# Performance work log

Hardware: AMD Instinct MI355X
Metric: run time of the kernel (lower is better)

## Reference

```python
import jax, jax.numpy as jnp
import numpy as np

# Norse-style LIF constants (LIFParameters defaults, method='super', alpha=100)
DT = 0.001
TAU_SYN_INV = 200.0
TAU_MEM_INV = 100.0
V_TH = 1.0
V_LEAK = 0.0
V_RESET = 0.0
ALPHA = 100.0

@jax.custom_vjp
def heaviside(x):
    return (x > 0).astype(x.dtype)

def _heaviside_fwd(x):
    return heaviside(x), x

def _heaviside_bwd(x, g):
    # SuperSpike surrogate: 1 / (alpha*|x| + 1)^2
    return (g / (ALPHA * jnp.abs(x) + 1.0) ** 2,)

heaviside.defvjp(_heaviside_fwd, _heaviside_bwd)

def lif_step(v, i, inp_cur):
    # explicit-Euler LIF: membrane decays toward leak driven by synaptic current,
    # synaptic current decays, spikes reset membrane, input arrives as current jump
    v_dec = v + DT * TAU_MEM_INV * ((V_LEAK - v) + i)
    i_dec = i * (1.0 - DT * TAU_SYN_INV)
    z = heaviside(v_dec - V_TH)
    v_new = (1.0 - z) * v_dec + z * V_RESET
    i_new = i_dec + inp_cur
    return z, v_new, i_new

def li_step(v, i, inp_cur):
    # leaky integrator (non-spiking readout)
    v_new = v + DT * TAU_MEM_INV * ((V_LEAK - v) + i)
    i_new = i * (1.0 - DT * TAU_SYN_INV) + inp_cur
    return v_new, i_new


def setup_inputs() -> dict:
    key = jax.random.key(0)
    k1, k2, k3 = jax.random.split(key, 3)
    T, B = 64, 128
    FS2, H1, HC, OC, OUT = 4096, 2048, 2, 4, 10
    spl1, spl2 = FS2 // HC, H1 // OC
    x = jax.random.uniform(k1, (T, B, FS2), dtype=jnp.float32)
    w_hidden = jax.random.normal(k2, (HC, spl1, H1), dtype=jnp.float32) / np.sqrt(spl1)
    w_out = jax.random.normal(k3, (OC, spl2, OUT), dtype=jnp.float32) / np.sqrt(spl2)
    return {"x": x, "w_hidden": w_hidden, "w_out": w_out}


def reference(x, w_hidden, w_out):
    T, B, FS2 = x.shape
    HC, SPL1, H1 = w_hidden.shape
    OC, SPL2, OUT = w_out.shape
    f32 = x.dtype

    def step(carry, x_t):
        vdh, idh, vsh, ish, vdo, ido, vso, iso = carry
        # split input across hidden dendritic channels: [HC, B, SPL1]
        zc = x_t.reshape(B, HC, SPL1).transpose(1, 0, 2)
        cur_h = jnp.einsum('cbi,cio->cbo', zc, w_hidden)      # [HC, B, H1]
        s_d, vdh, idh = lif_step(vdh, idh, cur_h)             # dendritic spikes
        z_s, vsh, ish = lif_step(vsh, ish, s_d.sum(0))        # somatic spikes [B, H1]
        # split hidden spikes across output dendritic channels: [OC, B, SPL2]
        zo = z_s.reshape(B, OC, SPL2).transpose(1, 0, 2)
        cur_o = jnp.einsum('cbi,cio->cbo', zo, w_out)         # [OC, B, OUT]
        s_o, vdo, ido = lif_step(vdo, ido, cur_o)
        vso, iso = li_step(vso, iso, s_o.sum(0))              # readout voltage [B, OUT]
        return (vdh, idh, vsh, ish, vdo, ido, vso, iso), vso

    z = jnp.zeros
    carry0 = (z((HC, B, H1), f32), z((HC, B, H1), f32),
              z((B, H1), f32), z((B, H1), f32),
              z((OC, B, OUT), f32), z((OC, B, OUT), f32),
              z((B, OUT), f32), z((B, OUT), f32))
    _, voltages = jax.lax.scan(step, carry0, x)
    return voltages  # [T, B, 10]
```

## Files before the change

### kernel.cpp

```cpp
#include <hip/hip_runtime.h>

#define B 128
#define HC 2
#define H1 2048
#define FS2 4096
#define NK 2048
#define OC 4
#define SPL2 512
#define NOUT 10
#define T 64
#define HBH (HC*B*H1)

typedef __attribute__((ext_vector_type(8))) short bf16x8;
typedef __attribute__((ext_vector_type(4))) float f32x4;

__device__ __forceinline__ unsigned short f2bf(float f) {
  unsigned u = __float_as_uint(f);
  u += 0x7fff + ((u >> 16) & 1);
  return (unsigned short)(u >> 16);
}
__device__ __forceinline__ float bf2f(unsigned short s) {
  return __uint_as_float(((unsigned)s) << 16);
}

__device__ __forceinline__ void gload16(const void* g, void* l) {
  __builtin_amdgcn_global_load_lds(
      (const __attribute__((address_space(1))) unsigned int*)g,
      (__attribute__((address_space(3))) unsigned int*)l, 16, 0, 0);
}

__global__ __launch_bounds__(256) void init_state(float* __restrict__ p, int n) {
  int i = blockIdx.x * 256 + threadIdx.x;
  if (i < n) p[i] = 0.f;
}

__global__ __launch_bounds__(256) void conv_x(
    const float4* __restrict__ xin, ushort4* __restrict__ xh,
    ushort4* __restrict__ xl, int n4) {
  for (int i = blockIdx.x * 256 + threadIdx.x; i < n4; i += gridDim.x * 256) {
    float4 v = xin[i];
    ushort4 h, lo;
    h.x = f2bf(v.x); h.y = f2bf(v.y); h.z = f2bf(v.z); h.w = f2bf(v.w);
    lo.x = f2bf(v.x - bf2f(h.x)); lo.y = f2bf(v.y - bf2f(h.y));
    lo.z = f2bf(v.z - bf2f(h.z)); lo.w = f2bf(v.w - bf2f(h.w));
    xh[i] = h; xl[i] = lo;
  }
}

__global__ __launch_bounds__(256) void conv_w(
    const float* __restrict__ w, unsigned short* __restrict__ wth,
    unsigned short* __restrict__ wtl) {
  __shared__ float s[64][65];
  const int c = blockIdx.z;
  const int n0 = blockIdx.x * 64, k0 = blockIdx.y * 64;
  const int tid = threadIdx.x;
  const int r = tid >> 4, c4 = (tid & 15) * 4;
#pragma unroll
  for (int q = 0; q < 4; ++q) {
    int kr = r + q * 16;
    float4 v = *(const float4*)(w + ((size_t)c * NK + k0 + kr) * H1 + n0 + c4);
    s[kr][c4 + 0] = v.x; s[kr][c4 + 1] = v.y;
    s[kr][c4 + 2] = v.z; s[kr][c4 + 3] = v.w;
  }
  __syncthreads();
#pragma unroll
  for (int q = 0; q < 4; ++q) {
    int nr = r + q * 16;
    float a0 = s[c4 + 0][nr], a1 = s[c4 + 1][nr];
    float a2 = s[c4 + 2][nr], a3 = s[c4 + 3][nr];
    ushort4 h, lo;
    h.x = f2bf(a0); h.y = f2bf(a1); h.z = f2bf(a2); h.w = f2bf(a3);
    lo.x = f2bf(a0 - bf2f(h.x)); lo.y = f2bf(a1 - bf2f(h.y));
    lo.z = f2bf(a2 - bf2f(h.z)); lo.w = f2bf(a3 - bf2f(h.w));
    size_t off = ((size_t)c * H1 + n0 + nr) * NK + k0 + c4;
    *(ushort4*)(wth + off) = h;
    *(ushort4*)(wtl + off) = lo;
  }
}

__global__ __launch_bounds__(512, 2) void gemm_split(
    const unsigned short* __restrict__ xh, const unsigned short* __restrict__ xl,
    const unsigned short* __restrict__ wth, const unsigned short* __restrict__ wtl,
    float* __restrict__ cur, int Mc, int nMblk) {
  const int bid = blockIdx.x;
  int c, nb, mb;
  if ((nMblk & 3) == 0) {
    const int xcd = bid & 7;
    const int slot = bid >> 3;
    c = xcd & 1;
    const int q = xcd >> 1;
    const int mq = nMblk >> 2;
    nb = slot & 7;
    mb = q * mq + (slot >> 3);
  } else {
    mb = bid % nMblk;
    int rest = bid / nMblk;
    nb = rest & 7;
    c = rest >> 3;
  }
  const int bm = mb * 256, bn = nb * 256;

  __shared__ unsigned short lds[65536];
  const int tid = threadIdx.x;

  unsigned dstOff[2]; size_t srcA[2], srcB[2];
#pragma unroll
  for (int q = 0; q < 2; ++q) {
    int idx = q * 512 + tid;
    int row = idx >> 2, ps = idx & 3;
    int ks = (ps - (row >> 1)) & 3;
    int ar = bm + row; if (ar > Mc - 1) ar = Mc - 1;
    srcA[q] = (size_t)ar * FS2 + (size_t)c * NK + ks * 8;
    srcB[q] = (size_t)c * NK * H1 + (size_t)(bn + row) * NK + ks * 8;
    dstOff[q] = idx * 8;
  }

  const int l = tid & 63, w = tid >> 6;
  const int wr = w >> 2, wc = w & 3;
  const int lrow = l & 15, lks = l >> 4;
  unsigned aoff[8], boff[4];
#pragma unroll
  for (int m = 0; m < 8; ++m) {
    int row = wr * 128 + m * 16 + lrow;
    int ps = (lks + (row >> 1)) & 3;
    aoff[m] = row * 32 + ps * 8;
  }
#pragma unroll
  for (int n = 0; n < 4; ++n) {
    int rn = wc * 64 + n * 16 + lrow;
    int ps = (lks + (rn >> 1)) & 3;
    boff[n] = rn * 32 + ps * 8;
  }

  f32x4 acc[8][4];
#pragma unroll
  for (int m = 0; m < 8; ++m)
#pragma unroll
    for (int n = 0; n < 4; ++n) acc[m][n] = (f32x4){0.f, 0.f, 0.f, 0.f};

  gload16(xh  + srcA[0], &lds[dstOff[0]]);
  gload16(xh  + srcA[1], &lds[dstOff[1]]);
  gload16(wth + srcB[0], &lds[16384 + dstOff[0]]);
  gload16(wth + srcB[1], &lds[16384 + dstOff[1]]);
  gload16(wtl + srcB[0], &lds[24576 + dstOff[0]]);
  gload16(wtl + srcB[1], &lds[24576 + dstOff[1]]);
  gload16(xl  + srcA[0], &lds[8192 + dstOff[0]]);
  gload16(xl  + srcA[1], &lds[8192 + dstOff[1]]);

  const int NT = NK / 32;
  for (int t = 0; t < NT - 1; ++t) {
    const unsigned cb   = (unsigned)(t & 1) * 32768;
    const unsigned nbuf = (unsigned)((t + 1) & 1) * 32768;
    const int kn = (t + 1) * 32;

    asm volatile("s_waitcnt vmcnt(4)\ns_barrier" ::: "memory");
    gload16(xh  + srcA[0] + kn, &lds[nbuf + dstOff[0]]);
    gload16(xh  + srcA[1] + kn, &lds[nbuf + dstOff[1]]);
    gload16(wth + srcB[0] + kn, &lds[nbuf + 16384 + dstOff[0]]);
    gload16(wth + srcB[1] + kn, &lds[nbuf + 16384 + dstOff[1]]);
    bf16x8 bh[4], ah[8];
#pragma unroll
    for (int n = 0; n < 4; ++n) bh[n] = *(const bf16x8*)&lds[cb + 16384 + boff[n]];
#pragma unroll
    for (int m = 0; m < 8; ++m) ah[m] = *(const bf16x8*)&lds[cb + aoff[m]];
    __builtin_amdgcn_s_setprio(1);
#pragma unroll
    for (int m = 0; m < 8; ++m)
#pragma unroll
      for (int n = 0; n < 4; ++n)
        acc[m][n] = __builtin_amdgcn_mfma_f32_16x16x32_bf16(ah[m], bh[n], acc[m][n], 0, 0, 0);
    __builtin_amdgcn_s_setprio(0);

    asm volatile("s_waitcnt vmcnt(6)\ns_barrier" ::: "memory");
    gload16(wtl + srcB[0] + kn, &lds[nbuf + 24576 + dstOff[0]]);
    gload16(wtl + srcB[1] + kn, &lds[nbuf + 24576 + dstOff[1]]);
    bf16x8 bl[4];
#pragma unroll
    for (int n = 0; n < 4; ++n) bl[n] = *(const bf16x8*)&lds[cb + 24576 + boff[n]];
    __builtin_amdgcn_s_setprio(1);
#pragma unroll
    for (int m = 0; m < 8; ++m)
#pragma unroll
      for (int n = 0; n < 4; ++n)
        acc[m][n] = __builtin_amdgcn_mfma_f32_16x16x32_bf16(ah[m], bl[n], acc[m][n], 0, 0, 0);
    __builtin_amdgcn_s_setprio(0);

    asm volatile("s_waitcnt vmcnt(6)\ns_barrier" ::: "memory");
    gload16(xl + srcA[0] + kn, &lds[nbuf + 8192 + dstOff[0]]);
    gload16(xl + srcA[1] + kn, &lds[nbuf + 8192 + dstOff[1]]);
    bf16x8 al[8];
#pragma unroll
    for (int m = 0; m < 8; ++m) al[m] = *(const bf16x8*)&lds[cb + 8192 + aoff[m]];
    __builtin_amdgcn_s_setprio(1);
#pragma unroll
    for (int m = 0; m < 8; ++m)
#pragma unroll
      for (int n = 0; n < 4; ++n)
        acc[m][n] = __builtin_amdgcn_mfma_f32_16x16x32_bf16(al[m], bh[n], acc[m][n], 0, 0, 0);
    __builtin_amdgcn_s_setprio(0);
  }

  {
    const unsigned cb = (unsigned)((NT - 1) & 1) * 32768;
    asm volatile("s_waitcnt vmcnt(4)\ns_barrier" ::: "memory");
    bf16x8 bh[4], ah[8];
#pragma unroll
    for (int n = 0; n < 4; ++n) bh[n] = *(const bf16x8*)&lds[cb + 16384 + boff[n]];
#pragma unroll
    for (int m = 0; m < 8; ++m) ah[m] = *(const bf16x8*)&lds[cb + aoff[m]];
#pragma unroll
    for (int m = 0; m < 8; ++m)
#pragma unroll
      for (int n = 0; n < 4; ++n)
        acc[m][n] = __builtin_amdgcn_mfma_f32_16x16x32_bf16(ah[m], bh[n], acc[m][n], 0, 0, 0);
    asm volatile("s_waitcnt vmcnt(2)\ns_barrier" ::: "memory");
    bf16x8 bl[4];
#pragma unroll
    for (int n = 0; n < 4; ++n) bl[n] = *(const bf16x8*)&lds[cb + 24576 + boff[n]];
#pragma unroll
    for (int m = 0; m < 8; ++m)
#pragma unroll
      for (int n = 0; n < 4; ++n)
        acc[m][n] = __builtin_amdgcn_mfma_f32_16x16x32_bf16(ah[m], bl[n], acc[m][n], 0, 0, 0);
    asm volatile("s_waitcnt vmcnt(0)\ns_barrier" ::: "memory");
    bf16x8 al[8];
#pragma unroll
    for (int m = 0; m < 8; ++m) al[m] = *(const bf16x8*)&lds[cb + 8192 + aoff[m]];
#pragma unroll
    for (int m = 0; m < 8; ++m)
#pragma unroll
      for (int n = 0; n < 4; ++n)
        acc[m][n] = __builtin_amdgcn_mfma_f32_16x16x32_bf16(al[m], bh[n], acc[m][n], 0, 0, 0);
  }

  float* Cc = cur + (size_t)c * Mc * H1;
#pragma unroll
  for (int m = 0; m < 8; ++m) {
    int grow = bm + wr * 128 + m * 16 + (l >> 4) * 4;
    if (grow < Mc) {
#pragma unroll
      for (int n = 0; n < 4; ++n) {
        int gcol = bn + wc * 64 + n * 16 + (l & 15);
        float* Cp = Cc + (size_t)grow * H1 + gcol;
        Cp[0]      = acc[m][n][0];
        Cp[H1]     = acc[m][n][1];
        Cp[2 * H1] = acc[m][n][2];
        Cp[3 * H1] = acc[m][n][3];
      }
    }
  }
}

__global__ __launch_bounds__(256) void seq_chunk(
    const float* __restrict__ cur, const float* __restrict__ wout,
    float* __restrict__ vdh, float* __restrict__ idh,
    float* __restrict__ vsh, float* __restrict__ ish,
    float* __restrict__ vdo, float* __restrict__ ido,
    float* __restrict__ sp_g, int t0, int tc, int Mc) {
  const int b = blockIdx.x >> 2;
  const int oc = blockIdx.x & 3;
  const int tid = threadIdx.x;
  __shared__ float wols[SPL2 * NOUT];
  __shared__ float zls[SPL2];
  __shared__ float cols[16];

#pragma unroll
  for (int q = 0; q < 5; ++q) {
    int i4 = q * 256 + tid;
    ((float4*)wols)[i4] = ((const float4*)(wout + (size_t)oc * SPL2 * NOUT))[i4];
  }
  const int hb = oc * SPL2;
  float vdl[HC][2], idl[HC][2], vsl[2], isl[2];
#pragma unroll
  for (int c = 0; c < HC; ++c)
#pragma unroll
    for (int u = 0; u < 2; ++u) {
      size_t o = ((size_t)c * B + b) * H1 + hb + tid + u * 256;
      vdl[c][u] = vdh[o]; idl[c][u] = idh[o];
    }
#pragma unroll
  for (int u = 0; u < 2; ++u) {
    size_t o = (size_t)b * H1 + hb + tid + u * 256;
    vsl[u] = vsh[o]; isl[u] = ish[o];
  }
  float vo = 0.f, io = 0.f;
  if (tid < NOUT) {
    vo = vdo[(oc * B + b) * NOUT + tid];
    io = ido[(oc * B + b) * NOUT + tid];
  }
  float pc[HC][2];
#pragma unroll
  for (int c = 0; c < HC; ++c)
#pragma unroll
    for (int u = 0; u < 2; ++u)
      pc[c][u] = cur[((size_t)c * Mc + b) * H1 + hb + tid + u * 256];

  for (int tl = 0; tl < tc; ++tl) {
#pragma unroll
    for (int u = 0; u < 2; ++u) {
      float zsum = 0.f;
#pragma unroll
      for (int c = 0; c < HC; ++c) {
        float v = vdl[c][u], i = idl[c][u];
        float vdec = v + 0.1f * (i - v);
        float idec = 0.8f * i;
        bool z = (vdec - 1.0f) > 0.f;
        vdl[c][u] = z ? 0.f : vdec;
        idl[c][u] = idec + pc[c][u];
        zsum += z ? 1.f : 0.f;
      }
      float v = vsl[u], i = isl[u];
      float vdec = v + 0.1f * (i - v);
      float idec = 0.8f * i;
      bool z = (vdec - 1.0f) > 0.f;
      vsl[u] = z ? 0.f : vdec;
      isl[u] = idec + zsum;
      zls[tid + u * 256] = z ? 1.f : 0.f;
    }
    if (tl + 1 < tc) {
#pragma unroll
      for (int c = 0; c < HC; ++c)
#pragma unroll
        for (int u = 0; u < 2; ++u)
          pc[c][u] = cur[((size_t)c * Mc + (tl + 1) * B + b) * H1 + hb + tid + u * 256];
    }
    __syncthreads();
    {
      const int g = tid >> 4, li = tid & 15;
      if (g < NOUT) {
        float s = 0.f;
#pragma unroll
        for (int j = 0; j < 32; ++j) {
          int i2 = li + 16 * j;
          s += zls[i2] * wols[i2 * NOUT + g];
        }
        s += __shfl_xor(s, 1); s += __shfl_xor(s, 2);
        s += __shfl_xor(s, 4); s += __shfl_xor(s, 8);
        if (li == 0) cols[g] = s;
      }
    }
    __syncthreads();
    if (tid < NOUT) {
      float vdec = vo + 0.1f * (io - vo);
      float idec = 0.8f * io;
      bool z = (vdec - 1.0f) > 0.f;
      vo = z ? 0.f : vdec;
      io = idec + cols[tid];
      sp_g[((size_t)(t0 + tl) * B + b) * (OC * NOUT) + oc * NOUT + tid] = z ? 1.f : 0.f;
    }
  }

#pragma unroll
  for (int c = 0; c < HC; ++c)
#pragma unroll
    for (int u = 0; u < 2; ++u) {
      size_t o = ((size_t)c * B + b) * H1 + hb + tid + u * 256;
      vdh[o] = vdl[c][u]; idh[o] = idl[c][u];
    }
#pragma unroll
  for (int u = 0; u < 2; ++u) {
    size_t o = (size_t)b * H1 + hb + tid + u * 256;
    vsh[o] = vsl[u]; ish[o] = isl[u];
  }
  if (tid < NOUT) {
    vdo[(oc * B + b) * NOUT + tid] = vo;
    ido[(oc * B + b) * NOUT + tid] = io;
  }
}

__global__ __launch_bounds__(256) void integrate_out(
    const float* __restrict__ sp_g, float* __restrict__ out) {
  int i = blockIdx.x * 256 + threadIdx.x;
  if (i >= B * NOUT) return;
  int b = i / NOUT, o = i % NOUT;
  float vr = 0.f, ir = 0.f;
  for (int t = 0; t < T; ++t) {
    const float* p = sp_g + ((size_t)(t * B + b) * OC) * NOUT + o;
    float ssum = ((p[0] + p[NOUT]) + p[2 * NOUT]) + p[3 * NOUT];
    float vn = vr + 0.1f * (ir - vr);
    ir = 0.8f * ir + ssum;
    vr = vn;
    out[(size_t)(t * B + b) * NOUT + o] = vn;
  }
}

extern "C" void kernel_launch(void* const* d_in, const int* in_sizes, int n_in,
                              void* d_out, int out_size, void* d_ws, size_t ws_size,
                              hipStream_t stream) {
  const float* x  = (const float*)d_in[0];
  const float* wh = (const float*)d_in[1];
  const float* wo = (const float*)d_in[2];
  float* out = (float*)d_out;
  char* ws = (char*)d_ws;

  unsigned short* wth = (unsigned short*)ws;
  unsigned short* wtl = wth + (size_t)HC * NK * H1;
  float* st  = (float*)(wtl + (size_t)HC * NK * H1);
  float* vdh = st;
  float* idh = vdh + HBH;
  float* vsh = idh + HBH;
  float* ish = vsh + (size_t)B * H1;
  float* vdo = ish + (size_t)B * H1;
  float* ido = vdo + OC * B * NOUT;
  float* sp_g = ido + OC * B * NOUT;
  float* dyn = sp_g + (size_t)T * B * OC * NOUT;
  const int NSTATE = (int)(sp_g - st);

  size_t fixed_bytes = (size_t)((char*)dyn - ws);
  size_t avail = (ws_size > fixed_bytes + 256) ? ws_size - fixed_bytes - 256 : 0;
  const size_t per_t = (size_t)HC * B * H1 * 4 + (size_t)B * FS2 * 2 * 2;
  int Tc = (int)(avail / per_t);
  if (Tc > T) Tc = T;
  if (Tc >= 2) Tc &= ~1;
  if (Tc < 1) Tc = 1;

  float* cur = dyn;
  unsigned short* xh = (unsigned short*)(cur + (size_t)Tc * HC * B * H1);
  unsigned short* xl = xh + (size_t)Tc * B * FS2;

  init_state<<<(NSTATE + 255) / 256, 256, 0, stream>>>(st, NSTATE);
  conv_w<<<dim3(H1 / 64, NK / 64, HC), 256, 0, stream>>>(wh, wth, wtl);

  for (int t0 = 0; t0 < T; t0 += Tc) {
    int tc = (T - t0 < Tc) ? (T - t0) : Tc;
    int Mc = tc * B;
    int n4 = Mc * (FS2 / 4);
    int cb = (n4 + 255) / 256; if (cb > 2048) cb = 2048;
    conv_x<<<cb, 256, 0, stream>>>((const float4*)(x + (size_t)t0 * B * FS2),
                                   (ushort4*)xh, (ushort4*)xl, n4);
    int nMblk = (Mc + 255) / 256;
    gemm_split<<<HC * 8 * nMblk, 512, 0, stream>>>(xh, xl, wth, wtl, cur, Mc, nMblk);
    seq_chunk<<<B * OC, 256, 0, stream>>>(cur, wo, vdh, idh, vsh, ish,
                                          vdo, ido, sp_g, t0, tc, Mc);
  }
  integrate_out<<<(B * NOUT + 255) / 256, 256, 0, stream>>>(sp_g, out);
}
```

Before: 427.5 us.

## Fuse fp32-to-bf16 split of activations into GEMM A-tile loading

Removes the separate conv_x kernel and has the GEMM read fp32 activations straight into registers, split them into hi/lo bf16 in-kernel, and write both halves into the LDS double buffer. This drops the xh/xl workspace round trip and one launch per chunk, and frees workspace so larger time chunks fit (Tc now rounded to multiples of 8). The cost is extra VALU conversion work and register pressure inside the GEMM, plus a restructured pipeline with explicit lgkmcnt waits and sched barriers. The lo half is now truncated rather than rounded.

```diff
diff --git a/kernel.cpp b/kernel.cpp
--- a/kernel.cpp
+++ b/kernel.cpp
@@ -32,19 +32,6 @@
 __global__ __launch_bounds__(256) void init_state(float* __restrict__ p, int n) {
   int i = blockIdx.x * 256 + threadIdx.x;
   if (i < n) p[i] = 0.f;
-}
-
-__global__ __launch_bounds__(256) void conv_x(
-    const float4* __restrict__ xin, ushort4* __restrict__ xh,
-    ushort4* __restrict__ xl, int n4) {
-  for (int i = blockIdx.x * 256 + threadIdx.x; i < n4; i += gridDim.x * 256) {
-    float4 v = xin[i];
-    ushort4 h, lo;
-    h.x = f2bf(v.x); h.y = f2bf(v.y); h.z = f2bf(v.z); h.w = f2bf(v.w);
-    lo.x = f2bf(v.x - bf2f(h.x)); lo.y = f2bf(v.y - bf2f(h.y));
-    lo.z = f2bf(v.z - bf2f(h.z)); lo.w = f2bf(v.w - bf2f(h.w));
-    xh[i] = h; xl[i] = lo;
-  }
 }
 
 __global__ __launch_bounds__(256) void conv_w(
@@ -79,7 +66,7 @@
 }
 
 __global__ __launch_bounds__(512, 2) void gemm_split(
-    const unsigned short* __restrict__ xh, const unsigned short* __restrict__ xl,
+    const float* __restrict__ xA,
     const unsigned short* __restrict__ wth, const unsigned short* __restrict__ wtl,
     float* __restrict__ cur, int Mc, int nMblk) {
   const int bid = blockIdx.x;
@@ -103,14 +90,14 @@
   __shared__ unsigned short lds[65536];
   const int tid = threadIdx.x;
 
-  unsigned dstOff[2]; size_t srcA[2], srcB[2];
+  unsigned dstOff[2]; size_t srcAf[2], srcB[2];
 #pragma unroll
   for (int q = 0; q < 2; ++q) {
     int idx = q * 512 + tid;
     int row = idx >> 2, ps = idx & 3;
     int ks = (ps - (row >> 1)) & 3;
     int ar = bm + row; if (ar > Mc - 1) ar = Mc - 1;
-    srcA[q] = (size_t)ar * FS2 + (size_t)c * NK + ks * 8;
+    srcAf[q] = (size_t)ar * FS2 + (size_t)c * NK + ks * 8;
     srcB[q] = (size_t)c * NK * H1 + (size_t)(bn + row) * NK + ks * 8;
     dstOff[q] = idx * 8;
   }
@@ -138,31 +125,64 @@
 #pragma unroll
     for (int n = 0; n < 4; ++n) acc[m][n] = (f32x4){0.f, 0.f, 0.f, 0.f};
 
-  gload16(xh  + srcA[0], &lds[dstOff[0]]);
-  gload16(xh  + srcA[1], &lds[dstOff[1]]);
-  gload16(wth + srcB[0], &lds[16384 + dstOff[0]]);
-  gload16(wth + srcB[1], &lds[16384 + dstOff[1]]);
-  gload16(wtl + srcB[0], &lds[24576 + dstOff[0]]);
-  gload16(wtl + srcB[1], &lds[24576 + dstOff[1]]);
-  gload16(xl  + srcA[0], &lds[8192 + dstOff[0]]);
-  gload16(xl  + srcA[1], &lds[8192 + dstOff[1]]);
+  float4 fa[2][2];
+
+#define LOAD_A(k0)                                                     \
+  do {                                                                 \
+    fa[0][0] = *(const float4*)(xA + srcAf[0] + (k0));                 \
+    fa[0][1] = *(const float4*)(xA + srcAf[0] + (k0) + 4);             \
+    fa[1][0] = *(const float4*)(xA + srcAf[1] + (k0));                 \
+    fa[1][1] = *(const float4*)(xA + srcAf[1] + (k0) + 4);             \
+  } while (0)
+#define STAGE_BH(bufbase, k0)                                          \
+  do {                                                                 \
+    gload16(wth + srcB[0] + (k0), &lds[(bufbase) + 16384 + dstOff[0]]);\
+    gload16(wth + srcB[1] + (k0), &lds[(bufbase) + 16384 + dstOff[1]]);\
+  } while (0)
+#define STAGE_BL(bufbase, k0)                                          \
+  do {                                                                 \
+    gload16(wtl + srcB[0] + (k0), &lds[(bufbase) + 24576 + dstOff[0]]);\
+    gload16(wtl + srcB[1] + (k0), &lds[(bufbase) + 24576 + dstOff[1]]);\
+  } while (0)
+#define CVT_WRITE(bufbase)                                             \
+  do {                                                                 \
+    _Pragma("unroll")                                                  \
+    for (int q = 0; q < 2; ++q) {                                      \
+      union { unsigned short s[8]; bf16x8 v; } hi, lo;                 \
+      const float* fp = (const float*)&fa[q][0];                       \
+      _Pragma("unroll")                                                \
+      for (int j = 0; j < 8; ++j) {                                    \
+        unsigned short h = f2bf(fp[j]);                                \
+        hi.s[j] = h;                                                   \
+        lo.s[j] = (unsigned short)(__float_as_uint(fp[j] - bf2f(h)) >> 16); \
+      }                                                                \
+      *(bf16x8*)&lds[(bufbase) + dstOff[q]] = hi.v;                    \
+      *(bf16x8*)&lds[(bufbase) + 8192 + dstOff[q]] = lo.v;             \
+    }                                                                  \
+  } while (0)
 
   const int NT = NK / 32;
-  for (int t = 0; t < NT - 1; ++t) {
+  LOAD_A(0);
+  STAGE_BH(0, 0);
+  STAGE_BL(0, 0);
+  asm volatile("s_waitcnt vmcnt(2)" ::: "memory");
+  CVT_WRITE(0);
+
+  for (int t = 0; t < NT; ++t) {
     const unsigned cb   = (unsigned)(t & 1) * 32768;
     const unsigned nbuf = (unsigned)((t + 1) & 1) * 32768;
+    const int pf = (t + 1 < NT);
     const int kn = (t + 1) * 32;
 
-    asm volatile("s_waitcnt vmcnt(4)\ns_barrier" ::: "memory");
-    gload16(xh  + srcA[0] + kn, &lds[nbuf + dstOff[0]]);
-    gload16(xh  + srcA[1] + kn, &lds[nbuf + dstOff[1]]);
-    gload16(wth + srcB[0] + kn, &lds[nbuf + 16384 + dstOff[0]]);
-    gload16(wth + srcB[1] + kn, &lds[nbuf + 16384 + dstOff[1]]);
+    asm volatile("s_waitcnt vmcnt(2) lgkmcnt(0)\ns_barrier" ::: "memory");
+    if (pf) { LOAD_A(kn); STAGE_BH(nbuf, kn); }
     bf16x8 bh[4], ah[8];
 #pragma unroll
     for (int n = 0; n < 4; ++n) bh[n] = *(const bf16x8*)&lds[cb + 16384 + boff[n]];
 #pragma unroll
     for (int m = 0; m < 8; ++m) ah[m] = *(const bf16x8*)&lds[cb + aoff[m]];
+    asm volatile("s_waitcnt lgkmcnt(0)" ::: "memory");
+    __builtin_amdgcn_sched_barrier(0);
     __builtin_amdgcn_s_setprio(1);
 #pragma unroll
     for (int m = 0; m < 8; ++m)
@@ -171,12 +191,14 @@
         acc[m][n] = __builtin_amdgcn_mfma_f32_16x16x32_bf16(ah[m], bh[n], acc[m][n], 0, 0, 0);
     __builtin_amdgcn_s_setprio(0);
 
-    asm volatile("s_waitcnt vmcnt(6)\ns_barrier" ::: "memory");
-    gload16(wtl + srcB[0] + kn, &lds[nbuf + 24576 + dstOff[0]]);
-    gload16(wtl + srcB[1] + kn, &lds[nbuf + 24576 + dstOff[1]]);
+    if (pf) asm volatile("s_waitcnt vmcnt(6)\ns_barrier" ::: "memory");
+    else    asm volatile("s_waitcnt vmcnt(0)\ns_barrier" ::: "memory");
+    if (pf) STAGE_BL(nbuf, kn);
     bf16x8 bl[4];
 #pragma unroll
     for (int n = 0; n < 4; ++n) bl[n] = *(const bf16x8*)&lds[cb + 24576 + boff[n]];
+    asm volatile("s_waitcnt lgkmcnt(0)" ::: "memory");
+    __builtin_amdgcn_sched_barrier(0);
     __builtin_amdgcn_s_setprio(1);
 #pragma unroll
     for (int m = 0; m < 8; ++m)
@@ -185,12 +207,11 @@
         acc[m][n] = __builtin_amdgcn_mfma_f32_16x16x32_bf16(ah[m], bl[n], acc[m][n], 0, 0, 0);
     __builtin_amdgcn_s_setprio(0);
 
-    asm volatile("s_waitcnt vmcnt(6)\ns_barrier" ::: "memory");
-    gload16(xl + srcA[0] + kn, &lds[nbuf + 8192 + dstOff[0]]);
-    gload16(xl + srcA[1] + kn, &lds[nbuf + 8192 + dstOff[1]]);
     bf16x8 al[8];
 #pragma unroll
     for (int m = 0; m < 8; ++m) al[m] = *(const bf16x8*)&lds[cb + 8192 + aoff[m]];
+    asm volatile("s_waitcnt lgkmcnt(0)" ::: "memory");
+    __builtin_amdgcn_sched_barrier(0);
     __builtin_amdgcn_s_setprio(1);
 #pragma unroll
     for (int m = 0; m < 8; ++m)
@@ -198,40 +219,15 @@
       for (int n = 0; n < 4; ++n)
         acc[m][n] = __builtin_amdgcn_mfma_f32_16x16x32_bf16(al[m], bh[n], acc[m][n], 0, 0, 0);
     __builtin_amdgcn_s_setprio(0);
-  }
-
-  {
-    const unsigned cb = (unsigned)((NT - 1) & 1) * 32768;
-    asm volatile("s_waitcnt vmcnt(4)\ns_barrier" ::: "memory");
-    bf16x8 bh[4], ah[8];
-#pragma unroll
-    for (int n = 0; n < 4; ++n) bh[n] = *(const bf16x8*)&lds[cb + 16384 + boff[n]];
-#pragma unroll
-    for (int m = 0; m < 8; ++m) ah[m] = *(const bf16x8*)&lds[cb + aoff[m]];
-#pragma unroll
-    for (int m = 0; m < 8; ++m)
-#pragma unroll
-      for (int n = 0; n < 4; ++n)
-        acc[m][n] = __builtin_amdgcn_mfma_f32_16x16x32_bf16(ah[m], bh[n], acc[m][n], 0, 0, 0);
-    asm volatile("s_waitcnt vmcnt(2)\ns_barrier" ::: "memory");
-    bf16x8 bl[4];
-#pragma unroll
-    for (int n = 0; n < 4; ++n) bl[n] = *(const bf16x8*)&lds[cb + 24576 + boff[n]];
-#pragma unroll
-    for (int m = 0; m < 8; ++m)
-#pragma unroll
-      for (int n = 0; n < 4; ++n)
-        acc[m][n] = __builtin_amdgcn_mfma_f32_16x16x32_bf16(ah[m], bl[n], acc[m][n], 0, 0, 0);
-    asm volatile("s_waitcnt vmcnt(0)\ns_barrier" ::: "memory");
-    bf16x8 al[8];
-#pragma unroll
-    for (int m = 0; m < 8; ++m) al[m] = *(const bf16x8*)&lds[cb + 8192 + aoff[m]];
-#pragma unroll
-    for (int m = 0; m < 8; ++m)
-#pragma unroll
-      for (int n = 0; n < 4; ++n)
-        acc[m][n] = __builtin_amdgcn_mfma_f32_16x16x32_bf16(al[m], bh[n], acc[m][n], 0, 0, 0);
-  }
+    if (pf) {
+      asm volatile("s_waitcnt vmcnt(2)" ::: "memory");
+      CVT_WRITE(nbuf);
+    }
+  }
+#undef LOAD_A
+#undef STAGE_BH
+#undef STAGE_BL
+#undef CVT_WRITE
 
   float* Cc = cur + (size_t)c * Mc * H1;
 #pragma unroll
@@ -408,15 +404,14 @@
 
   size_t fixed_bytes = (size_t)((char*)dyn - ws);
   size_t avail = (ws_size > fixed_bytes + 256) ? ws_size - fixed_bytes - 256 : 0;
-  const size_t per_t = (size_t)HC * B * H1 * 4 + (size_t)B * FS2 * 2 * 2;
+  const size_t per_t = (size_t)HC * B * H1 * 4;
   int Tc = (int)(avail / per_t);
   if (Tc > T) Tc = T;
-  if (Tc >= 2) Tc &= ~1;
+  if (Tc >= 8) Tc &= ~7;
+  else if (Tc >= 2) Tc &= ~1;
   if (Tc < 1) Tc = 1;
 
   float* cur = dyn;
-  unsigned short* xh = (unsigned short*)(cur + (size_t)Tc * HC * B * H1);
-  unsigned short* xl = xh + (size_t)Tc * B * FS2;
 
   init_state<<<(NSTATE + 255) / 256, 256, 0, stream>>>(st, NSTATE);
   conv_w<<<dim3(H1 / 64, NK / 64, HC), 256, 0, stream>>>(wh, wth, wtl);
@@ -424,12 +419,9 @@
   for (int t0 = 0; t0 < T; t0 += Tc) {
     int tc = (T - t0 < Tc) ? (T - t0) : Tc;
     int Mc = tc * B;
-    int n4 = Mc * (FS2 / 4);
-    int cb = (n4 + 255) / 256; if (cb > 2048) cb = 2048;
-    conv_x<<<cb, 256, 0, stream>>>((const float4*)(x + (size_t)t0 * B * FS2),
-                                   (ushort4*)xh, (ushort4*)xl, n4);
     int nMblk = (Mc + 255) / 256;
-    gemm_split<<<HC * 8 * nMblk, 512, 0, stream>>>(xh, xl, wth, wtl, cur, Mc, nMblk);
+    gemm_split<<<HC * 8 * nMblk, 512, 0, stream>>>(
+        x + (size_t)t0 * B * FS2, wth, wtl, cur, Mc, nMblk);
     seq_chunk<<<B * OC, 256, 0, stream>>>(cur, wo, vdh, idh, vsh, ish,
                                           vdo, ido, sp_g, t0, tc, Mc);
   }
```

Result: no change. 434.2 us (+1.6%).
